# Performance work log

Hardware: AMD Instinct MI355X
Metric: run time of the kernel (lower is better)

## Reference

```python
import jax, jax.numpy as jnp
import numpy as np

N, IN_DIM, HID, M, T, E, A, OUT = 10000, 256, 256, 8, 3, 160000, 2000, 10
LN_EPS = 1e-5


def _layernorm(x, g, b):
    mu = x.mean(-1, keepdims=True)
    var = ((x - mu) ** 2).mean(-1, keepdims=True)
    return (x - mu) * jax.lax.rsqrt(var + LN_EPS) * g + b


def _gcn_conv(x, w, b, src, dst, n):
    # PyG GCNConv: x' = D^{-1/2}(A+I)D^{-1/2} (x W) + b, deg counted on dst with self-loops
    xw = x @ w  # [n, out]
    loops = jnp.arange(n, dtype=src.dtype)
    s = jnp.concatenate([src, loops])
    d = jnp.concatenate([dst, loops])
    deg = jax.ops.segment_sum(jnp.ones(d.shape[0], xw.dtype), d, num_segments=n)
    dinv = jax.lax.rsqrt(jnp.maximum(deg, 1.0))
    norm = dinv[s] * dinv[d]
    out = jax.ops.segment_sum(xw[s] * norm[:, None], d, num_segments=n)
    return out + b


def setup_inputs() -> dict:
    key = jax.random.key(0)
    ks = jax.random.split(key, 26)
    g = lambda i, shape: (jax.random.normal(ks[i], shape, jnp.float32) * 0.02)
    return {
        "edge_index_t": jax.random.randint(ks[0], (T, 2, E), 0, N),
        "node_t": jax.random.randint(ks[1], (T, A), 0, N),
        "m": M,
        "emb": g(2, (N, IN_DIM)),
        "gcn_w1": g(3, (IN_DIM, HID)), "gcn_b1": jnp.zeros((HID,), jnp.float32),
        "gcn_w2": g(4, (HID, HID)), "gcn_b2": jnp.zeros((HID,), jnp.float32),
        "ln1_g": jnp.ones((HID,), jnp.float32), "ln1_b": jnp.zeros((HID,), jnp.float32),
        "tok_w1": g(5, (M, M)), "tok_b1": jnp.zeros((M,), jnp.float32),
        "tok_w2": g(6, (M, M)), "tok_b2": jnp.zeros((M,), jnp.float32),
        "ln2_g": jnp.ones((HID,), jnp.float32), "ln2_b": jnp.zeros((HID,), jnp.float32),
        "ch_w1": g(7, (HID, HID)), "ch_b1": jnp.zeros((HID,), jnp.float32),
        "ch_w2": g(8, (HID, HID)), "ch_b2": jnp.zeros((HID,), jnp.float32),
        "pred_w": g(9, (HID, HID)), "pred_b": jnp.zeros((HID,), jnp.float32),
        "cls1_w": g(10, (HID, HID)), "cls1_b": jnp.zeros((HID,), jnp.float32),
        "cls2_w": g(11, (HID, OUT)), "cls2_b": jnp.zeros((OUT,), jnp.float32),
    }


def reference(edge_index_t, node_t, m, emb,
              gcn_w1, gcn_b1, gcn_w2, gcn_b2,
              ln1_g, ln1_b, tok_w1, tok_b1, tok_w2, tok_b2,
              ln2_g, ln2_b, ch_w1, ch_b1, ch_w2, ch_b2,
              pred_w, pred_b, cls1_w, cls1_b, cls2_w, cls2_b):
    n = emb.shape[0]

    def mixer(xm):  # [n, m, hid]
        y = _layernorm(xm, ln1_g, ln1_b)
        # token MLP over the m axis (transpose(1,2) in torch)
        y = jnp.einsum('nmh,mk->nkh', y, tok_w1) + tok_b1[None, :, None]
        y = jax.nn.gelu(y, approximate=False)
        y = jnp.einsum('nmh,mk->nkh', y, tok_w2) + tok_b2[None, :, None]
        x = xm + y
        z = _layernorm(x, ln2_g, ln2_b)
        z = jax.nn.gelu(z @ ch_w1 + ch_b1, approximate=False) @ ch_w2 + ch_b2
        return x + z

    def step(x_m, inp):
        src, dst, nid = inp
        # forecast from current window (before this step's graph update)
        x_new = mixer(x_m).mean(axis=1)  # discrete FinalProcessLayer: mean over tokens
        # 2-layer GCN on the (shared) initial embeddings
        x = _gcn_conv(emb, gcn_w1, gcn_b1, src, dst, n)
        x = jax.nn.relu(x)
        x = _gcn_conv(x, gcn_w2, gcn_b2, src, dst, n)
        # boolean-mask scatter: zero rows of nodes listed in node_t[i]
        x = x.at[nid].set(0.0)
        x_m = jnp.concatenate([x_m[:, 1:, :], x[:, None, :]], axis=1)
        return x_m, x_new

    x_m0 = jnp.zeros((n, m, HID), emb.dtype)
    _, v = jax.lax.scan(step, x_m0, (edge_index_t[:, 0], edge_index_t[:, 1], node_t))
    # InvariantPredictor over all T timesteps at once: v [T, n, hid]
    h = jnp.tanh(v @ pred_w + pred_b)
    y_hat = jax.nn.relu((h @ cls1_w + cls1_b) @ cls2_w + cls2_b)
    return h, y_hat
```

## Files before the change

kernel.cpp:

```cpp
#include <hip/hip_runtime.h>
#include <math.h>

#define NN 10000
#define HIDD 256
#define MTOK 8
#define TT 3
#define EE 160000
#define AA 2000
#define OUTD 10
#define LNEPS 1e-5f

typedef unsigned short u16;
typedef __attribute__((ext_vector_type(8))) __bf16 bf16x8;
typedef __attribute__((ext_vector_type(4))) float f32x4;

__device__ __forceinline__ float gelu_f(float x) {
    return 0.5f * x * (1.f + erff(x * 0.7071067811865475f));
}
__device__ __forceinline__ u16 f2bf(float x) {
    unsigned u = __builtin_bit_cast(unsigned, x);
    return (u16)((u + 0x7FFFu + ((u >> 16) & 1u)) >> 16);
}
__device__ __forceinline__ float bf2f(u16 b) {
    return __builtin_bit_cast(float, (unsigned)b << 16);
}
__device__ __forceinline__ void gload16(const void* g, void* l) {
    __builtin_amdgcn_global_load_lds(
        (const __attribute__((address_space(1))) unsigned int*)g,
        (__attribute__((address_space(3))) unsigned int*)l, 16, 0, 0);
}

__global__ void count_kernel(const int* __restrict__ edge, int* __restrict__ cnt) {
    int g = blockIdx.y;
    const int* dst = edge + (size_t)g * 2 * EE + EE;
    int e = blockIdx.x * 256 + threadIdx.x;
    if (e < EE) atomicAdd(&cnt[g * NN + dst[e]], 1);
}

__global__ __launch_bounds__(1024) void scan_kernel(const int* __restrict__ cnt_all,
        int* __restrict__ rowstart_all, int* __restrict__ cursor_all, float* __restrict__ dinv_all) {
    int g = blockIdx.x;
    const int* cnt = cnt_all + (size_t)g * NN;
    int* rowstart = rowstart_all + (size_t)g * NN;
    int* cursor = cursor_all + (size_t)g * NN;
    float* dinv = dinv_all + (size_t)g * NN;
    __shared__ int wsum[16];
    int tid = threadIdx.x, lane = tid & 63, wid = tid >> 6;
    int carry = 0;
    for (int base = 0; base < NN; base += 1024) {
        int i = base + tid;
        int v = (i < NN) ? cnt[i] : 0;
        int s = v;
        #pragma unroll
        for (int o = 1; o < 64; o <<= 1) {
            int t = __shfl_up(s, o, 64);
            if (lane >= o) s += t;
        }
        if (lane == 63) wsum[wid] = s;
        __syncthreads();
        if (wid == 0) {
            int ws = (lane < 16) ? wsum[lane] : 0;
            #pragma unroll
            for (int o = 1; o < 16; o <<= 1) {
                int t = __shfl_up(ws, o, 64);
                if (lane >= o) ws += t;
            }
            if (lane < 16) wsum[lane] = ws;
        }
        __syncthreads();
        int woff = (wid > 0) ? wsum[wid - 1] : 0;
        int tot = wsum[15];
        if (i < NN) {
            int excl = carry + s + woff - v;
            rowstart[i] = excl;
            cursor[i] = excl;
            dinv[i] = rsqrtf((float)(v + 1));
        }
        carry += tot;
        __syncthreads();
    }
}

__global__ void fill_kernel(const int* __restrict__ edge, int* __restrict__ cursor, int* __restrict__ esrc) {
    int g = blockIdx.y;
    const int* src = edge + (size_t)g * 2 * EE;
    const int* dst = src + EE;
    int e = blockIdx.x * 256 + threadIdx.x;
    if (e < EE) {
        int d = dst[e];
        int idx = atomicAdd(&cursor[g * NN + d], 1);
        esrc[(size_t)g * EE + idx] = src[e];
    }
}

template<int RELU, int WF32, int WSPLIT>
__global__ __launch_bounds__(256) void gcn_agg(const float* __restrict__ xw, size_t xw_goff,
        const int* __restrict__ esrc_all, const int* __restrict__ rowstart_all,
        const int* __restrict__ cnt_all, const float* __restrict__ dinv_all,
        const float* __restrict__ bias, float* __restrict__ out,
        u16* __restrict__ ohi, u16* __restrict__ olo) {
    int g = blockIdx.y;
    const float* xwg = xw + (size_t)g * xw_goff;
    const int* esrc = esrc_all + (size_t)g * EE;
    const int* rowstart = rowstart_all + (size_t)g * NN;
    const int* cntp = cnt_all + (size_t)g * NN;
    const float* dinv = dinv_all + (size_t)g * NN;
    int wave = threadIdx.x >> 6, lane = threadIdx.x & 63;
    int d = blockIdx.x * 4 + wave;
    if (d >= NN) return;
    int start = rowstart[d];
    int len = cntp[d];
    float dd = dinv[d];
    int h = lane * 4;
    float4 a = *(const float4*)&xwg[(size_t)d * HIDD + h];
    float4 acc, accB;
    acc.x = a.x * dd; acc.y = a.y * dd; acc.z = a.z * dd; acc.w = a.w * dd;
    accB.x = 0.f; accB.y = 0.f; accB.z = 0.f; accB.w = 0.f;
    int i = 0;
    for (; i + 2 <= len; i += 2) {
        int s0 = esrc[start + i];
        int s1 = esrc[start + i + 1];
        float d0 = dinv[s0];
        float d1 = dinv[s1];
        float4 b0 = *(const float4*)&xwg[(size_t)s0 * HIDD + h];
        float4 b1 = *(const float4*)&xwg[(size_t)s1 * HIDD + h];
        acc.x = fmaf(b0.x, d0, acc.x);  accB.x = fmaf(b1.x, d1, accB.x);
        acc.y = fmaf(b0.y, d0, acc.y);  accB.y = fmaf(b1.y, d1, accB.y);
        acc.z = fmaf(b0.z, d0, acc.z);  accB.z = fmaf(b1.z, d1, accB.z);
        acc.w = fmaf(b0.w, d0, acc.w);  accB.w = fmaf(b1.w, d1, accB.w);
    }
    if (i < len) {
        int s0 = esrc[start + i];
        float d0 = dinv[s0];
        float4 b0 = *(const float4*)&xwg[(size_t)s0 * HIDD + h];
        acc.x = fmaf(b0.x, d0, acc.x);
        acc.y = fmaf(b0.y, d0, acc.y);
        acc.z = fmaf(b0.z, d0, acc.z);
        acc.w = fmaf(b0.w, d0, acc.w);
    }
    acc.x += accB.x; acc.y += accB.y; acc.z += accB.z; acc.w += accB.w;
    float o0 = acc.x * dd + bias[h + 0];
    float o1 = acc.y * dd + bias[h + 1];
    float o2 = acc.z * dd + bias[h + 2];
    float o3 = acc.w * dd + bias[h + 3];
    if (RELU) {
        o0 = fmaxf(o0, 0.f); o1 = fmaxf(o1, 0.f); o2 = fmaxf(o2, 0.f); o3 = fmaxf(o3, 0.f);
    }
    size_t obase = (size_t)g * NN * HIDD + (size_t)d * HIDD + h;
    if (WF32) {
        float4 o; o.x = o0; o.y = o1; o.z = o2; o.w = o3;
        *(float4*)&out[obase] = o;
    }
    if (WSPLIT) {
        ushort4 hv, lv;
        u16 h0 = f2bf(o0), h1 = f2bf(o1), h2 = f2bf(o2), h3 = f2bf(o3);
        hv.x = h0; hv.y = h1; hv.z = h2; hv.w = h3;
        lv.x = f2bf(o0 - bf2f(h0)); lv.y = f2bf(o1 - bf2f(h1));
        lv.z = f2bf(o2 - bf2f(h2)); lv.w = f2bf(o3 - bf2f(h3));
        *(ushort4*)&ohi[obase] = hv;
        *(ushort4*)&olo[obase] = lv;
    }
}

__global__ void mask_kernel(const int* __restrict__ node_t, float* __restrict__ xs) {
    int g = blockIdx.y;
    int node = node_t[(size_t)g * AA + blockIdx.x];
    xs[(size_t)g * NN * HIDD + (size_t)node * HIDD + threadIdx.x] = 0.f;
}

__global__ void split_kernel(const float* __restrict__ x, u16* __restrict__ hi, u16* __restrict__ lo, int n) {
    int i = blockIdx.x * 256 + threadIdx.x;
    if (i < n) {
        float v = x[i];
        u16 h = f2bf(v);
        hi[i] = h;
        lo[i] = f2bf(v - bf2f(h));
    }
}

__global__ void wsplit_all(const float* __restrict__ w0, const float* __restrict__ w1,
        const float* __restrict__ w2, const float* __restrict__ w3,
        const float* __restrict__ w4, const float* __restrict__ w5, u16* __restrict__ bt) {
    const float* W[6] = { w0, w1, w2, w3, w4, w5 };
    const float* Wm = W[blockIdx.y];
    u16* Bt = bt + (size_t)blockIdx.y * 256 * 768;
    int c = blockIdx.x, k = threadIdx.x;
    float x = Wm[k * 256 + c];
    u16 hi = f2bf(x), lo = f2bf(x - bf2f(hi));
    Bt[c * 768 + k] = hi;
    Bt[c * 768 + 256 + k] = hi;
    Bt[c * 768 + 512 + k] = lo;
}

template<int ACT, int WF32, int WSPLIT, int EPI>
__global__ __launch_bounds__(256) void gemm_split(
        const u16* __restrict__ Ahi, const u16* __restrict__ Alo,
        const u16* __restrict__ Bt, const float* __restrict__ bias,
        float* __restrict__ outf, u16* __restrict__ ohi, u16* __restrict__ olo,
        const float* __restrict__ xsum, int R) {
    __shared__ __align__(16) u16 ldsAhi[2][128 * 64];
    __shared__ __align__(16) u16 ldsAlo[128 * 64];
    __shared__ __align__(16) u16 ldsB[2][128 * 64];
    int tid = threadIdx.x;
    int lane = tid & 63, w = tid >> 6;
    int nwg = gridDim.x, orig = blockIdx.x;
    int xcd = orig & 7, i8 = orig >> 3;
    int q = nwg >> 3, r = nwg & 7;
    int bid = (xcd < r ? xcd * (q + 1) : r * (q + 1) + (xcd - r) * q) + i8;
    int rowbase = (bid >> 1) * 128;
    int cb = bid & 1;
    int wrow = (w >> 1) * 64, wcol = (w & 1) * 64;
    f32x4 acc[4][4];
    #pragma unroll
    for (int i = 0; i < 4; i++)
        #pragma unroll
        for (int j = 0; j < 4; j++) acc[i][j] = f32x4{0.f, 0.f, 0.f, 0.f};

    auto stageAhi = [&](int slot, int k) {
        int koff = k * 64;
        #pragma unroll
        for (int i = 0; i < 4; i++) {
            int j = i * 256 + tid;
            int rr = j >> 3, sl = j & 7;
            int grow = rowbase + rr; if (grow > R - 1) grow = R - 1;
            const u16* gp = Ahi + (size_t)grow * 256 + koff + ((sl ^ (rr & 7)) << 3);
            gload16(gp, &ldsAhi[slot][(i * 256 + (tid & 192)) << 3]);
        }
    };
    auto stageAlo = [&](int k) {
        int koff = k * 64;
        #pragma unroll
        for (int i = 0; i < 4; i++) {
            int j = i * 256 + tid;
            int rr = j >> 3, sl = j & 7;
            int grow = rowbase + rr; if (grow > R - 1) grow = R - 1;
            const u16* gp = Alo + (size_t)grow * 256 + koff + ((sl ^ (rr & 7)) << 3);
            gload16(gp, &ldsAlo[(i * 256 + (tid & 192)) << 3]);
        }
    };
    auto stageB = [&](int buf, int c) {
        #pragma unroll
        for (int i = 0; i < 4; i++) {
            int j = i * 256 + tid;
            int rr = j >> 3, sl = j & 7;
            const u16* gp = Bt + (size_t)(cb * 128 + rr) * 768 + c * 64 + ((sl ^ (rr & 7)) << 3);
            gload16(gp, &ldsB[buf][(i * 256 + (tid & 192)) << 3]);
        }
    };

    stageAhi(0, 0);
    stageAlo(0);
    stageB(0, 0);
    #pragma unroll
    for (int k = 0; k < 4; k++) {
        int sh = k & 1;
        stageB(1, 8 + k);
        asm volatile("s_waitcnt vmcnt(4)" ::: "memory");
        __builtin_amdgcn_s_barrier();
        __builtin_amdgcn_sched_barrier(0);
        __builtin_amdgcn_s_setprio(1);
        #pragma unroll
        for (int ks = 0; ks < 2; ks++) {
            bf16x8 ah[4], al[4], b[4];
            #pragma unroll
            for (int rf = 0; rf < 4; rf++) {
                int rr = wrow + rf * 16 + (lane & 15);
                int slot = (lane >> 4) + ks * 4;
                int offi = (rr << 6) + ((slot ^ (rr & 7)) << 3);
                ah[rf] = *(const bf16x8*)&ldsAhi[sh][offi];
                al[rf] = *(const bf16x8*)&ldsAlo[offi];
            }
            #pragma unroll
            for (int cf = 0; cf < 4; cf++) {
                int cc = wcol + cf * 16 + (lane & 15);
                int slot = (lane >> 4) + ks * 4;
                b[cf] = *(const bf16x8*)&ldsB[0][(cc << 6) + ((slot ^ (cc & 7)) << 3)];
            }
            #pragma unroll
            for (int rf = 0; rf < 4; rf++)
                #pragma unroll
                for (int cf = 0; cf < 4; cf++) {
                    acc[rf][cf] = __builtin_amdgcn_mfma_f32_16x16x32_bf16(ah[rf], b[cf], acc[rf][cf], 0, 0, 0);
                    acc[rf][cf] = __builtin_amdgcn_mfma_f32_16x16x32_bf16(al[rf], b[cf], acc[rf][cf], 0, 0, 0);
                }
        }
        __builtin_amdgcn_s_setprio(0);
        __builtin_amdgcn_sched_barrier(0);
        __builtin_amdgcn_s_barrier();
        if (k < 3) {
            stageAhi(sh ^ 1, k + 1);
            stageAlo(k + 1);
            stageB(0, k + 1);
            asm volatile("s_waitcnt vmcnt(12)" ::: "memory");
        } else {
            asm volatile("s_waitcnt vmcnt(0)" ::: "memory");
        }
        __builtin_amdgcn_s_barrier();
        __builtin_amdgcn_sched_barrier(0);
        __builtin_amdgcn_s_setprio(1);
        #pragma unroll
        for (int ks = 0; ks < 2; ks++) {
            bf16x8 a[4], b[4];
            #pragma unroll
            for (int rf = 0; rf < 4; rf++) {
                int rr = wrow + rf * 16 + (lane & 15);
                int slot = (lane >> 4) + ks * 4;
                a[rf] = *(const bf16x8*)&ldsAhi[sh][(rr << 6) + ((slot ^ (rr & 7)) << 3)];
            }
            #pragma unroll
            for (int cf = 0; cf < 4; cf++) {
                int cc = wcol + cf * 16 + (lane & 15);
                int slot = (lane >> 4) + ks * 4;
                b[cf] = *(const bf16x8*)&ldsB[1][(cc << 6) + ((slot ^ (cc & 7)) << 3)];
            }
            #pragma unroll
            for (int rf = 0; rf < 4; rf++)
                #pragma unroll
                for (int cf = 0; cf < 4; cf++)
                    acc[rf][cf] = __builtin_amdgcn_mfma_f32_16x16x32_bf16(a[rf], b[cf], acc[rf][cf], 0, 0, 0);
        }
        __builtin_amdgcn_s_setprio(0);
        __builtin_amdgcn_sched_barrier(0);
        __builtin_amdgcn_s_barrier();
    }
    #pragma unroll
    for (int rf = 0; rf < 4; rf++) {
        #pragma unroll
        for (int cf = 0; cf < 4; cf++) {
            int col = cb * 128 + wcol + cf * 16 + (lane & 15);
            float bv = bias[col];
            f32x4 v = acc[rf][cf];
            if (EPI == 1) {
                float s = 0.f;
                #pragma unroll
                for (int r2 = 0; r2 < 4; r2++) s += gelu_f(v[r2] + bv);
                float o = __shfl_xor(s, 16, 64);
                float nodesum = s + o;
                if (((lane >> 4) & 1) == 0) {
                    int node = ((rowbase + wrow + rf * 16) >> 3) + ((lane >> 4) >> 1);
                    u16 hi = f2bf(nodesum), lo = f2bf(nodesum - bf2f(hi));
                    ohi[(size_t)node * 256 + col] = hi;
                    olo[(size_t)node * 256 + col] = lo;
                }
            } else {
                int row0 = rowbase + wrow + rf * 16 + ((lane >> 4) << 2);
                #pragma unroll
                for (int r2 = 0; r2 < 4; r2++) {
                    int row = row0 + r2;
                    if (row < R) {
                        float val = v[r2] + bv;
                        if (ACT == 1) val = gelu_f(val);
                        if (ACT == 2) val = tanhf(val);
                        if (WF32) outf[(size_t)row * 256 + col] = val;
                        if (WSPLIT) {
                            u16 hi = f2bf(val), lo = f2bf(val - bf2f(hi));
                            ohi[(size_t)row * 256 + col] = hi;
                            olo[(size_t)row * 256 + col] = lo;
                        }
                    }
                }
            }
        }
    }
}

__global__ __launch_bounds__(512, 2) void tail_fused(
        const u16* __restrict__ s2_hi, const u16* __restrict__ s2_lo,
        const float* __restrict__ xsum,
        const u16* __restrict__ Bt_cw2, const float* __restrict__ cb2,
        const u16* __restrict__ Bt_pred, const float* __restrict__ pred_b,
        const u16* __restrict__ Bt_cls1, const float* __restrict__ cls1_b,
        const float* __restrict__ cls2_w, const float* __restrict__ cls2_b,
        float* __restrict__ h_out1, float* __restrict__ y_out1, int R) {
    __shared__ __align__(16) u16 ldsA[2][32 * 256];
    __shared__ __align__(16) u16 ldsB[256 * 64];
    int tid = threadIdx.x;
    int lane = tid & 63, wid = tid >> 6;
    int wrow = (wid & 1) * 16, wcol = (wid >> 1) * 64;
    int rowbase = blockIdx.x * 32;

    constexpr int KCH[12]  = {0,4,1,5,2,6,3,7,8,9,10,11};
    constexpr int BNEW[12] = {1,0,1,0,1,0,1,0,1,1,1,1};

    auto stageB = [&](int c, const u16* Bt) {
        #pragma unroll
        for (int i = 0; i < 4; i++) {
            int j = i * 512 + tid;
            int cc = j >> 3, sl = j & 7;
            const u16* gp = Bt + (size_t)cc * 768 + c * 64 + ((sl ^ (cc & 7)) << 3);
            gload16(gp, &ldsB[(i * 512 + (tid & 448)) << 3]);
        }
    };
    #pragma unroll
    for (int seg = 0; seg < 2; seg++) {
        const u16* src = seg ? s2_lo : s2_hi;
        #pragma unroll
        for (int i = 0; i < 2; i++) {
            int j = i * 512 + tid;
            int rr = j >> 5;
            int gch = (j >> 3) & 3, t = j & 7;
            int rowG = rowbase + rr; if (rowG > R - 1) rowG = R - 1;
            const u16* gp = src + (size_t)rowG * 256 + gch * 64 + ((t ^ (rr & 7)) << 3);
            gload16(gp, &ldsA[seg][(i * 512 + (tid & 448)) << 3]);
        }
    }

    for (int s = 0; s < 3; s++) {
        const u16* Bt = (s == 0) ? Bt_cw2 : (s == 1) ? Bt_pred : Bt_cls1;
        f32x4 acc[4];
        #pragma unroll
        for (int i = 0; i < 4; i++) acc[i] = f32x4{0.f, 0.f, 0.f, 0.f};
        #pragma unroll
        for (int p = 0; p < 12; p++) {
            if (BNEW[p]) {
                asm volatile("s_waitcnt lgkmcnt(0)" ::: "memory");
                __builtin_amdgcn_s_barrier();
                stageB(KCH[p], Bt);
                asm volatile("s_waitcnt vmcnt(0)" ::: "memory");
                __builtin_amdgcn_s_barrier();
            }
            __builtin_amdgcn_sched_barrier(0);
            __builtin_amdgcn_s_setprio(1);
            int c = KCH[p];
            int seg = (c >= 4 && c < 8) ? 1 : 0;
            int kbase = (c & 3) * 64;
            #pragma unroll
            for (int ks = 0; ks < 2; ks++) {
                int rr = wrow + (lane & 15);
                int slot = (lane >> 4) + ks * 4;
                bf16x8 a = *(const bf16x8*)&ldsA[seg][rr * 256 + kbase + ((slot ^ (rr & 7)) << 3)];
                #pragma unroll
                for (int cf = 0; cf < 4; cf++) {
                    int cc = wcol + cf * 16 + (lane & 15);
                    bf16x8 b = *(const bf16x8*)&ldsB[cc * 64 + ((slot ^ (cc & 7)) << 3)];
                    acc[cf] = __builtin_amdgcn_mfma_f32_16x16x32_bf16(a, b, acc[cf], 0, 0, 0);
                }
            }
            __builtin_amdgcn_s_setprio(0);
            __builtin_amdgcn_sched_barrier(0);
        }
        __builtin_amdgcn_s_barrier();
        #pragma unroll
        for (int cf = 0; cf < 4; cf++) {
            int col = wcol + cf * 16 + (lane & 15);
            #pragma unroll
            for (int r2 = 0; r2 < 4; r2++) {
                int row = wrow + ((lane >> 4) << 2) + r2;
                int rowG = rowbase + row;
                int rowC = rowG > R - 1 ? R - 1 : rowG;
                float av = acc[cf][r2];
                int pos = row * 256 + (col >> 6) * 64 + ((((col >> 3) & 7) ^ (row & 7)) << 3) + (col & 7);
                if (s == 0) {
                    float val = (xsum[(size_t)rowC * 256 + col] + av + 8.f * cb2[col]) * 0.125f;
                    u16 hi = f2bf(val), lo = f2bf(val - bf2f(hi));
                    ldsA[0][pos] = hi;
                    ldsA[1][pos] = lo;
                } else if (s == 1) {
                    float h = tanhf(av + pred_b[col]);
                    if (rowG < R) h_out1[(size_t)rowG * 256 + col] = h;
                    u16 hi = f2bf(h), lo = f2bf(h - bf2f(hi));
                    ldsA[0][pos] = hi;
                    ldsA[1][pos] = lo;
                } else {
                    ((float*)ldsA)[row * 256 + (col ^ (row & 31))] = av + cls1_b[col];
                }
            }
        }
    }
    float* w2 = (float*)ldsB;
    for (int i = tid; i < 256 * OUTD; i += 512) w2[i] = cls2_w[i];
    asm volatile("s_waitcnt lgkmcnt(0) vmcnt(0)" ::: "memory");
    __builtin_amdgcn_s_barrier();
    const float* gbuf = (const float*)ldsA;
    for (int o = tid; o < 32 * OUTD; o += 512) {
        int row = o / OUTD, j = o - row * OUTD;
        int rowG = rowbase + row;
        if (rowG < R) {
            float a2 = 0.f;
            for (int k = 0; k < 256; k++) a2 = fmaf(gbuf[row * 256 + (k ^ (row & 31))], w2[k * OUTD + j], a2);
            y_out1[(size_t)rowG * OUTD + j] = fmaxf(a2 + cls2_b[j], 0.f);
        }
    }
}

__global__ __launch_bounds__(256) void mixer_front(
        const float* __restrict__ xs, int nodebase,
        const float* __restrict__ ln1_g, const float* __restrict__ ln1_b,
        const float* __restrict__ tw1, const float* __restrict__ tb1,
        const float* __restrict__ tw2, const float* __restrict__ tb2,
        const float* __restrict__ ln2_g, const float* __restrict__ ln2_b,
        u16* __restrict__ z_hi, u16* __restrict__ z_lo, float* __restrict__ xsum_out) {
    int nv = nodebase + blockIdx.x;
    int step = nv >= NN ? 1 : 0;
    int n = nv - step * NN;
    const float* p1 = xs + ((size_t)step * NN + n) * HIDD;
    const float* p2 = step ? xs + (size_t)n * HIDD : nullptr;
    int tid = threadIdx.x;
    int wave = tid >> 6, lane = tid & 63;
    __shared__ __align__(16) float sx[MTOK][HIDD];
    __shared__ float stw1h[16], stw2[64], stb1[8], stb2[8], sw1s6[8];
    __shared__ float red[MTOK][2];
    if (tid < 16) stw1h[tid] = tw1[48 + tid];
    if (tid < 64) stw2[tid] = tw2[tid];
    if (tid < 8) {
        stb1[tid] = tb1[tid]; stb2[tid] = tb2[tid];
        float s = 0.f;
        #pragma unroll
        for (int m = 0; m < 6; m++) s += tw1[m * MTOK + tid];
        sw1s6[tid] = s;
    }
    sx[6][tid] = p2 ? p2[tid] : 0.f;
    sx[7][tid] = p1[tid];
    __syncthreads();
    float g1v = ln1_g[tid], b1v = ln1_b[tid];
    if (wave < 2) {
        int m = 6 + wave;
        float x0 = sx[m][lane], x1 = sx[m][lane + 64], x2 = sx[m][lane + 128], x3 = sx[m][lane + 192];
        float s = x0 + x1 + x2 + x3;
        float ss = x0 * x0 + x1 * x1 + x2 * x2 + x3 * x3;
        for (int off = 32; off > 0; off >>= 1) { s += __shfl_down(s, off, 64); ss += __shfl_down(ss, off, 64); }
        if (lane == 0) {
            float mu = s * (1.f / HIDD);
            float var = ss * (1.f / HIDD) - mu * mu;
            red[m][0] = mu;
            red[m][1] = rsqrtf(var + LNEPS);
        }
    }
    __syncthreads();
    float x6 = sx[6][tid], x7 = sx[7][tid];
    float ty6 = (x6 - red[6][0]) * red[6][1] * g1v + b1v;
    float ty7 = (x7 - red[7][0]) * red[7][1] * g1v + b1v;
    float u[MTOK];
    #pragma unroll
    for (int k = 0; k < MTOK; k++) {
        float a = stb1[k];
        a = fmaf(b1v, sw1s6[k], a);
        a = fmaf(ty6, stw1h[k], a);
        a = fmaf(ty7, stw1h[8 + k], a);
        u[k] = gelu_f(a);
    }
    float xsm = 0.f;
    #pragma unroll
    for (int k = 0; k < MTOK; k++) {
        float a = stb2[k];
        #pragma unroll
        for (int m = 0; m < MTOK; m++) a = fmaf(u[m], stw2[m * MTOK + k], a);
        if (k == 6) a += x6;
        if (k == 7) a += x7;
        sx[k][tid] = a;
        xsm += a;
    }
    xsum_out[(size_t)nv * HIDD + tid] = xsm;
    __syncthreads();
    float g2v = ln2_g[tid], b2v = ln2_b[tid];
    #pragma unroll
    for (int rep = 0; rep < 2; rep++) {
        int m = wave + rep * 4;
        float x0 = sx[m][lane], x1 = sx[m][lane + 64], x2 = sx[m][lane + 128], x3 = sx[m][lane + 192];
        float s = x0 + x1 + x2 + x3;
        float ss = x0 * x0 + x1 * x1 + x2 * x2 + x3 * x3;
        for (int off = 32; off > 0; off >>= 1) { s += __shfl_down(s, off, 64); ss += __shfl_down(ss, off, 64); }
        if (lane == 0) {
            float mu = s * (1.f / HIDD);
            float var = ss * (1.f / HIDD) - mu * mu;
            red[m][0] = mu;
            red[m][1] = rsqrtf(var + LNEPS);
        }
    }
    __syncthreads();
    #pragma unroll
    for (int m = 0; m < MTOK; m++) {
        float z = (sx[m][tid] - red[m][0]) * red[m][1] * g2v + b2v;
        u16 hi = f2bf(z), lo = f2bf(z - bf2f(hi));
        size_t idx = ((size_t)blockIdx.x * MTOK + m) * HIDD + tid;
        z_hi[idx] = hi;
        z_lo[idx] = lo;
    }
}

__global__ __launch_bounds__(256) void mixer_kernel(
        const float* __restrict__ ln1_g, const float* __restrict__ ln1_b,
        const float* __restrict__ tw1, const float* __restrict__ tb1,
        const float* __restrict__ tw2, const float* __restrict__ tb2,
        const float* __restrict__ ln2_g, const float* __restrict__ ln2_b,
        const float* __restrict__ cw1, const float* __restrict__ cb1,
        const float* __restrict__ cw2, const float* __restrict__ cb2,
        float* __restrict__ vout) {
    int tid = threadIdx.x;
    __shared__ __align__(16) float sx[MTOK][HIDD];
    __shared__ __align__(16) float sy[MTOK][HIDD];
    __shared__ float stw1[64], stw2[64], stb1[8], stb2[8];
    if (tid < 64) { stw1[tid] = tw1[tid]; stw2[tid] = tw2[tid]; }
    if (tid < 8)  { stb1[tid] = tb1[tid]; stb2[tid] = tb2[tid]; }
    __syncthreads();
    float b1v = ln1_b[tid];
    float ty[MTOK];
    #pragma unroll
    for (int m = 0; m < MTOK; m++) ty[m] = b1v;
    float u[MTOK];
    #pragma unroll
    for (int k = 0; k < MTOK; k++) {
        float a = stb1[k];
        #pragma unroll
        for (int m = 0; m < MTOK; m++) a = fmaf(ty[m], stw1[m * MTOK + k], a);
        u[k] = gelu_f(a);
    }
    #pragma unroll
    for (int k = 0; k < MTOK; k++) {
        float a = stb2[k];
        #pragma unroll
        for (int m = 0; m < MTOK; m++) a = fmaf(u[m], stw2[m * MTOK + k], a);
        sx[k][tid] = a;
    }
    __syncthreads();
    __shared__ float red[MTOK][2];
    int wave = tid >> 6, lane = tid & 63;
    float g2v = ln2_g[tid], b2v = ln2_b[tid];
    #pragma unroll
    for (int rep = 0; rep < 2; rep++) {
        int m = wave + rep * 4;
        float x0 = sx[m][lane], x1 = sx[m][lane + 64], x2 = sx[m][lane + 128], x3 = sx[m][lane + 192];
        float s = x0 + x1 + x2 + x3;
        float ss = x0 * x0 + x1 * x1 + x2 * x2 + x3 * x3;
        for (int off = 32; off > 0; off >>= 1) { s += __shfl_down(s, off, 64); ss += __shfl_down(ss, off, 64); }
        if (lane == 0) {
            float mu = s * (1.f / HIDD);
            float var = ss * (1.f / HIDD) - mu * mu;
            red[m][0] = mu;
            red[m][1] = rsqrtf(var + LNEPS);
        }
    }
    __syncthreads();
    #pragma unroll
    for (int m = 0; m < MTOK; m++) sy[m][tid] = (sx[m][tid] - red[m][0]) * red[m][1] * g2v + b2v;
    __syncthreads();
    float acc[MTOK];
    #pragma unroll
    for (int m = 0; m < MTOK; m++) acc[m] = 0.f;
    for (int h = 0; h < HIDD; h += 4) {
        float w0 = cw1[(h + 0) * HIDD + tid];
        float w1 = cw1[(h + 1) * HIDD + tid];
        float w2 = cw1[(h + 2) * HIDD + tid];
        float w3 = cw1[(h + 3) * HIDD + tid];
        #pragma unroll
        for (int m = 0; m < MTOK; m++) {
            const float4 a = *(const float4*)&sy[m][h];
            acc[m] = fmaf(a.x, w0, acc[m]);
            acc[m] = fmaf(a.y, w1, acc[m]);
            acc[m] = fmaf(a.z, w2, acc[m]);
            acc[m] = fmaf(a.w, w3, acc[m]);
        }
    }
    __syncthreads();
    float cb1v = cb1[tid];
    #pragma unroll
    for (int m = 0; m < MTOK; m++) sy[m][tid] = gelu_f(acc[m] + cb1v);
    __syncthreads();
    float acc2[MTOK];
    #pragma unroll
    for (int m = 0; m < MTOK; m++) acc2[m] = 0.f;
    for (int h = 0; h < HIDD; h += 4) {
        float w0 = cw2[(h + 0) * HIDD + tid];
        float w1 = cw2[(h + 1) * HIDD + tid];
        float w2 = cw2[(h + 2) * HIDD + tid];
        float w3 = cw2[(h + 3) * HIDD + tid];
        #pragma unroll
        for (int m = 0; m < MTOK; m++) {
            const float4 a = *(const float4*)&sy[m][h];
            acc2[m] = fmaf(a.x, w0, acc2[m]);
            acc2[m] = fmaf(a.y, w1, acc2[m]);
            acc2[m] = fmaf(a.z, w2, acc2[m]);
            acc2[m] = fmaf(a.w, w3, acc2[m]);
        }
    }
    float cb2v = cb2[tid];
    float ssum = 0.f;
    #pragma unroll
    for (int m = 0; m < MTOK; m++) ssum += sx[m][tid] + acc2[m] + cb2v;
    vout[tid] = ssum * (1.f / MTOK);
}

__global__ __launch_bounds__(256) void t0_head(const float* __restrict__ v0row,
        const float* __restrict__ pred_w, const float* __restrict__ pred_b,
        const float* __restrict__ cls1_w, const float* __restrict__ cls1_b,
        const float* __restrict__ cls2_w, const float* __restrict__ cls2_b,
        float* __restrict__ h0row, float* __restrict__ y0row) {
    __shared__ float s[HIDD], s2[HIDD];
    int tid = threadIdx.x;
    s[tid] = v0row[tid];
    __syncthreads();
    float a = 0.f;
    for (int k = 0; k < HIDD; k++) a = fmaf(s[k], pred_w[k * HIDD + tid], a);
    float h = tanhf(a + pred_b[tid]);
    h0row[tid] = h;
    s2[tid] = h;
    __syncthreads();
    a = 0.f;
    for (int k = 0; k < HIDD; k++) a = fmaf(s2[k], cls1_w[k * HIDD + tid], a);
    float g = a + cls1_b[tid];
    __syncthreads();
    s[tid] = g;
    __syncthreads();
    if (tid < OUTD) {
        float y = 0.f;
        for (int k = 0; k < HIDD; k++) y = fmaf(s[k], cls2_w[k * OUTD + tid], y);
        y0row[tid] = fmaxf(y + cls2_b[tid], 0.f);
    }
}

__global__ void bcast_both(const float* __restrict__ h0row, const float* __restrict__ y0row,
        float* __restrict__ hout, float* __restrict__ yout) {
    int n = blockIdx.x, tid = threadIdx.x;
    hout[(size_t)n * HIDD + tid] = h0row[tid];
    if (tid < OUTD) yout[(size_t)n * OUTD + tid] = y0row[tid];
}

extern "C" void kernel_launch(void* const* d_in, const int* in_sizes, int n_in,
                              void* d_out, int out_size, void* d_ws, size_t ws_size,
                              hipStream_t stream) {
    const int* edge    = (const int*)d_in[0];
    const int* node_t  = (const int*)d_in[1];
    const float* emb   = (const float*)d_in[3];
    const float* gcn_w1 = (const float*)d_in[4];
    const float* gcn_b1 = (const float*)d_in[5];
    const float* gcn_w2 = (const float*)d_in[6];
    const float* gcn_b2 = (const float*)d_in[7];
    const float* ln1_g = (const float*)d_in[8];
    const float* ln1_b = (const float*)d_in[9];
    const float* tw1   = (const float*)d_in[10];
    const float* tb1   = (const float*)d_in[11];
    const float* tw2   = (const float*)d_in[12];
    const float* tb2   = (const float*)d_in[13];
    const float* ln2_g = (const float*)d_in[14];
    const float* ln2_b = (const float*)d_in[15];
    const float* cw1   = (const float*)d_in[16];
    const float* cb1   = (const float*)d_in[17];
    const float* cw2   = (const float*)d_in[18];
    const float* cb2   = (const float*)d_in[19];
    const float* pred_w = (const float*)d_in[20];
    const float* pred_b = (const float*)d_in[21];
    const float* cls1_w = (const float*)d_in[22];
    const float* cls1_b = (const float*)d_in[23];
    const float* cls2_w = (const float*)d_in[24];
    const float* cls2_b = (const float*)d_in[25];

    const size_t NH = (size_t)NN * HIDD;
    char* wsb = (char*)d_ws;
    size_t off = 0;
    auto alloc = [&](size_t bytes) { char* p = wsb + off; off = (off + bytes + 255) & ~(size_t)255; return p; };
    float* xs   = (float*)alloc(2 * NH * 4);
    u16* v_hi   = (u16*)alloc(2 * NH * 2);
    u16* v_lo   = (u16*)alloc(2 * NH * 2);
    u16* h_hi   = (u16*)alloc(2 * NH * 2);
    u16* h_lo   = (u16*)alloc(2 * NH * 2);
    float* xw2  = (float*)alloc(2 * NH * 4);
    float* xsum = (float*)alloc(2 * NH * 4);
    u16* Bt_all = (u16*)alloc((size_t)6 * 256 * 768 * 2);
    u16* Bt_cw1  = Bt_all;
    u16* Bt_cw2  = Bt_all + 1 * 256 * 768;
    u16* Bt_pred = Bt_all + 2 * 256 * 768;
    u16* Bt_cls1 = Bt_all + 3 * 256 * 768;
    u16* Bt_gw1  = Bt_all + 4 * 256 * 768;
    u16* Bt_gw2  = Bt_all + 5 * 256 * 768;
    float* dinv  = (float*)alloc(2 * NN * 4);
    float* zeros = (float*)alloc(HIDD * 4);
    float* v0row = (float*)alloc(HIDD * 4);
    float* h0row = (float*)alloc(HIDD * 4);
    float* y0row = (float*)alloc(16 * 4);
    int* cnt    = (int*)alloc(2 * NN * 4);
    int* rowst  = (int*)alloc(2 * NN * 4);
    int* cursor = (int*)alloc(2 * NN * 4);
    int* esrc   = (int*)alloc((size_t)2 * EE * 4);
    float* xw    = (float*)h_hi;
    u16*  emb_hi = h_lo;
    u16*  emb_lo = h_lo + NH;
    u16*  agg_hi = v_hi;
    u16*  agg_lo = v_lo;
    u16*  s2_hi  = (u16*)xw2;
    u16*  s2_lo  = (u16*)xw2 + 2 * NH;
    size_t remain = (ws_size > off + 4096) ? (ws_size - off - 4096) : 0;
    int CHN = (int)(remain / 8192);
    if (CHN > 2 * NN) CHN = 2 * NN;
    CHN &= ~15;
    if (CHN < 16) CHN = 16;
    const size_t ZE = (size_t)CHN * MTOK * HIDD;
    u16* z_hi  = (u16*)alloc(ZE * 2);
    u16* z_lo  = (u16*)alloc(ZE * 2);

    float* h_out = (float*)d_out;
    float* y_out = h_out + (size_t)TT * NH;

    hipMemsetAsync(zeros, 0, HIDD * sizeof(float), stream);
    wsplit_all<<<dim3(256, 6), 256, 0, stream>>>(cw1, cw2, pred_w, cls1_w, gcn_w1, gcn_w2, Bt_all);
    split_kernel<<<(NN * HIDD + 255) / 256, 256, 0, stream>>>(emb, emb_hi, emb_lo, NN * HIDD);
    gemm_split<0, 1, 0, 0><<<2 * ((NN + 127) / 128), 256, 0, stream>>>(
        emb_hi, emb_lo, Bt_gw1, zeros, xw, nullptr, nullptr, nullptr, NN);

    mixer_kernel<<<1, 256, 0, stream>>>(ln1_g, ln1_b, tw1, tb1, tw2, tb2,
        ln2_g, ln2_b, cw1, cb1, cw2, cb2, v0row);
    t0_head<<<1, 256, 0, stream>>>(v0row, pred_w, pred_b, cls1_w, cls1_b,
        cls2_w, cls2_b, h0row, y0row);
    bcast_both<<<NN, 256, 0, stream>>>(h0row, y0row, h_out, y_out);

    hipMemsetAsync(cnt, 0, 2 * NN * sizeof(int), stream);
    count_kernel<<<dim3((EE + 255) / 256, 2), 256, 0, stream>>>(edge, cnt);
    scan_kernel<<<2, 1024, 0, stream>>>(cnt, rowst, cursor, dinv);
    fill_kernel<<<dim3((EE + 255) / 256, 2), 256, 0, stream>>>(edge, cursor, esrc);
    gcn_agg<1, 0, 1><<<dim3((NN + 3) / 4, 2), 256, 0, stream>>>(xw, 0,
        esrc, rowst, cnt, dinv, gcn_b1, nullptr, agg_hi, agg_lo);
    gemm_split<0, 1, 0, 0><<<2 * ((2 * NN + 127) / 128), 256, 0, stream>>>(
        agg_hi, agg_lo, Bt_gw2, zeros, xw2, nullptr, nullptr, nullptr, 2 * NN);
    gcn_agg<0, 1, 0><<<dim3((NN + 3) / 4, 2), 256, 0, stream>>>(xw2, NH,
        esrc, rowst, cnt, dinv, gcn_b2, xs, nullptr, nullptr);
    mask_kernel<<<dim3(AA, 2), 256, 0, stream>>>(node_t, xs);

    for (int nb = 0; nb < 2 * NN; nb += CHN) {
        int nodes = 2 * NN - nb < CHN ? 2 * NN - nb : CHN;
        int R = nodes * MTOK;
        int rb = (R + 127) / 128;
        mixer_front<<<nodes, 256, 0, stream>>>(xs, nb,
            ln1_g, ln1_b, tw1, tb1, tw2, tb2, ln2_g, ln2_b, z_hi, z_lo, xsum);
        gemm_split<1, 0, 0, 1><<<2 * rb, 256, 0, stream>>>(
            z_hi, z_lo, Bt_cw1, cb1, nullptr,
            s2_hi + (size_t)nb * HIDD, s2_lo + (size_t)nb * HIDD, nullptr, R);
    }
    tail_fused<<<(2 * NN + 31) / 32, 512, 0, stream>>>(
        s2_hi, s2_lo, xsum,
        Bt_cw2, cb2, Bt_pred, pred_b, Bt_cls1, cls1_b, cls2_w, cls2_b,
        h_out + NH, y_out + (size_t)NN * OUTD, 2 * NN);
}
```

Before: 499.3 us.

## Unroll GCN gather by four, remap tail blocks per XCD, vectorize z stores

The GCN aggregation loop now handles four edges per iteration with four independent accumulators, so more gather loads are in flight at once. The tail_fused kernel remaps its block indices so consecutive row tiles land on the same XCD, which should improve L2 locality. The LN2 output stage writes normalized values back to LDS and then stores the bf16 hi/lo pairs as 16-byte vectors instead of scalar u16 stores. The costs are extra registers and an added barrier.

After: 499.2 us (median of 3 runs). No clear change (-0.0%).

```diff
diff --git a/kernel.cpp b/kernel.cpp
--- a/kernel.cpp
+++ b/kernel.cpp
@@ -13,6 +13,7 @@
 typedef unsigned short u16;
 typedef __attribute__((ext_vector_type(8))) __bf16 bf16x8;
 typedef __attribute__((ext_vector_type(4))) float f32x4;
+typedef __attribute__((ext_vector_type(8))) unsigned short u16x8;
 
 __device__ __forceinline__ float gelu_f(float x) {
     return 0.5f * x * (1.f + erff(x * 0.7071067811865475f));
@@ -113,32 +114,44 @@
     float dd = dinv[d];
     int h = lane * 4;
     float4 a = *(const float4*)&xwg[(size_t)d * HIDD + h];
-    float4 acc, accB;
-    acc.x = a.x * dd; acc.y = a.y * dd; acc.z = a.z * dd; acc.w = a.w * dd;
-    accB.x = 0.f; accB.y = 0.f; accB.z = 0.f; accB.w = 0.f;
+    float4 a0, a1, a2, a3;
+    a0.x = a.x * dd; a0.y = a.y * dd; a0.z = a.z * dd; a0.w = a.w * dd;
+    a1.x = 0.f; a1.y = 0.f; a1.z = 0.f; a1.w = 0.f;
+    a2 = a1; a3 = a1;
     int i = 0;
-    for (; i + 2 <= len; i += 2) {
+    for (; i + 4 <= len; i += 4) {
         int s0 = esrc[start + i];
         int s1 = esrc[start + i + 1];
-        float d0 = dinv[s0];
-        float d1 = dinv[s1];
+        int s2 = esrc[start + i + 2];
+        int s3 = esrc[start + i + 3];
+        float d0 = dinv[s0], d1 = dinv[s1], d2 = dinv[s2], d3 = dinv[s3];
         float4 b0 = *(const float4*)&xwg[(size_t)s0 * HIDD + h];
         float4 b1 = *(const float4*)&xwg[(size_t)s1 * HIDD + h];
-        acc.x = fmaf(b0.x, d0, acc.x);  accB.x = fmaf(b1.x, d1, accB.x);
-        acc.y = fmaf(b0.y, d0, acc.y);  accB.y = fmaf(b1.y, d1, accB.y);
-        acc.z = fmaf(b0.z, d0, acc.z);  accB.z = fmaf(b1.z, d1, accB.z);
-        acc.w = fmaf(b0.w, d0, acc.w);  accB.w = fmaf(b1.w, d1, accB.w);
-    }
-    if (i < len) {
+        float4 b2 = *(const float4*)&xwg[(size_t)s2 * HIDD + h];
+        float4 b3 = *(const float4*)&xwg[(size_t)s3 * HIDD + h];
+        a0.x = fmaf(b0.x, d0, a0.x); a1.x = fmaf(b1.x, d1, a1.x);
+        a2.x = fmaf(b2.x, d2, a2.x); a3.x = fmaf(b3.x, d3, a3.x);
+        a0.y = fmaf(b0.y, d0, a0.y); a1.y = fmaf(b1.y, d1, a1.y);
+        a2.y = fmaf(b2.y, d2, a2.y); a3.y = fmaf(b3.y, d3, a3.y);
+        a0.z = fmaf(b0.z, d0, a0.z); a1.z = fmaf(b1.z, d1, a1.z);
+        a2.z = fmaf(b2.z, d2, a2.z); a3.z = fmaf(b3.z, d3, a3.z);
+        a0.w = fmaf(b0.w, d0, a0.w); a1.w = fmaf(b1.w, d1, a1.w);
+        a2.w = fmaf(b2.w, d2, a2.w); a3.w = fmaf(b3.w, d3, a3.w);
+    }
+    for (; i < len; i++) {
         int s0 = esrc[start + i];
         float d0 = dinv[s0];
         float4 b0 = *(const float4*)&xwg[(size_t)s0 * HIDD + h];
-        acc.x = fmaf(b0.x, d0, acc.x);
-        acc.y = fmaf(b0.y, d0, acc.y);
-        acc.z = fmaf(b0.z, d0, acc.z);
-        acc.w = fmaf(b0.w, d0, acc.w);
-    }
-    acc.x += accB.x; acc.y += accB.y; acc.z += accB.z; acc.w += accB.w;
+        a0.x = fmaf(b0.x, d0, a0.x);
+        a0.y = fmaf(b0.y, d0, a0.y);
+        a0.z = fmaf(b0.z, d0, a0.z);
+        a0.w = fmaf(b0.w, d0, a0.w);
+    }
+    float4 acc;
+    acc.x = (a0.x + a1.x) + (a2.x + a3.x);
+    acc.y = (a0.y + a1.y) + (a2.y + a3.y);
+    acc.z = (a0.z + a1.z) + (a2.z + a3.z);
+    acc.w = (a0.w + a1.w) + (a2.w + a3.w);
     float o0 = acc.x * dd + bias[h + 0];
     float o1 = acc.y * dd + bias[h + 1];
     float o2 = acc.z * dd + bias[h + 2];
@@ -377,7 +390,11 @@
     int tid = threadIdx.x;
     int lane = tid & 63, wid = tid >> 6;
     int wrow = (wid & 1) * 16, wcol = (wid >> 1) * 64;
-    int rowbase = blockIdx.x * 32;
+    int nwg = gridDim.x, orig = blockIdx.x;
+    int xcd = orig & 7, i8 = orig >> 3;
+    int q = nwg >> 3, r = nwg & 7;
+    int bidx = (xcd < r ? xcd * (q + 1) : r * (q + 1) + (xcd - r) * q) + i8;
+    int rowbase = bidx * 32;
 
     constexpr int KCH[12]  = {0,4,1,5,2,6,3,7,8,9,10,11};
     constexpr int BNEW[12] = {1,0,1,0,1,0,1,0,1,1,1,1};
@@ -571,10 +588,23 @@
     #pragma unroll
     for (int m = 0; m < MTOK; m++) {
         float z = (sx[m][tid] - red[m][0]) * red[m][1] * g2v + b2v;
-        u16 hi = f2bf(z), lo = f2bf(z - bf2f(hi));
-        size_t idx = ((size_t)blockIdx.x * MTOK + m) * HIDD + tid;
-        z_hi[idx] = hi;
-        z_lo[idx] = lo;
+        sx[m][tid] = z;
+    }
+    __syncthreads();
+    {
+        int m = tid >> 5;
+        int c0 = (tid & 31) << 3;
+        u16x8 hv, lv;
+        #pragma unroll
+        for (int j = 0; j < 8; j++) {
+            float z = sx[m][c0 + j];
+            u16 h = f2bf(z);
+            hv[j] = h;
+            lv[j] = f2bf(z - bf2f(h));
+        }
+        size_t base = ((size_t)blockIdx.x * MTOK + m) * HIDD + c0;
+        *(u16x8*)&z_hi[base] = hv;
+        *(u16x8*)&z_lo[base] = lv;
     }
 }
 
```
